# Performance work log

Measured on AMD Instinct MI355X. Metric: run time of the kernel, lower is better.

Reference implementation:

```python
import jax, jax.numpy as jnp
import numpy as np

N, E, IN_C, OUT_C, HEADS = 50000, 800000, 256, 256, 4
C = OUT_C // HEADS  # per-head channels = 64
BN_EPS = 1e-5


def setup_inputs() -> dict:
    key = jax.random.key(0)
    ks = jax.random.split(key, 16)
    inp = {
        'x': jax.random.normal(ks[0], (N, IN_C), dtype=jnp.float32),
        'edge_index': jax.random.randint(ks[1], (2, E), 0, N, dtype=jnp.int64),
        'edge_attr': jax.random.uniform(ks[2], (E, 1), dtype=jnp.float32),
        'spatial_coords': jax.random.normal(ks[3], (N, 2), dtype=jnp.float32),
        # GATConv params
        'W_gat': jax.random.normal(ks[4], (IN_C, HEADS * C), dtype=jnp.float32) * 0.05,
        'att_src': jax.random.normal(ks[5], (HEADS, C), dtype=jnp.float32) * 0.05,
        'att_dst': jax.random.normal(ks[6], (HEADS, C), dtype=jnp.float32) * 0.05,
        'bias_gat': jnp.zeros((HEADS * C,), dtype=jnp.float32),
        # spatial_attention MLP (computed but unused by the original forward)
        'w1': jax.random.normal(ks[7], (1, 64), dtype=jnp.float32) * 0.05,
        'b1': jnp.zeros((64,), dtype=jnp.float32),
        'w2': jax.random.normal(ks[8], (64, HEADS), dtype=jnp.float32) * 0.05,
        'b2': jnp.zeros((HEADS,), dtype=jnp.float32),
        # feature_transform: Linear + BatchNorm1d (eval stats) + ReLU (+Dropout=identity)
        'w_ft': jax.random.normal(ks[9], (IN_C, OUT_C), dtype=jnp.float32) * 0.05,
        'b_ft': jnp.zeros((OUT_C,), dtype=jnp.float32),
        'bn_gamma': jnp.ones((OUT_C,), dtype=jnp.float32),
        'bn_beta': jnp.zeros((OUT_C,), dtype=jnp.float32),
        'bn_mean': jax.random.normal(ks[10], (OUT_C,), dtype=jnp.float32) * 0.01,
        'bn_var': jax.random.uniform(ks[11], (OUT_C,), dtype=jnp.float32, minval=0.5, maxval=1.5),
    }
    return inp


def _forward(x, edge_index, edge_attr, W_gat, att_src, att_dst, bias_gat,
             w1, b1, w2, b2, w_ft, b_ft, bn_gamma, bn_beta, bn_mean, bn_var):
    n = x.shape[0]
    # add self-loops (PyG GATConv default)
    loop = jnp.arange(n, dtype=edge_index.dtype)
    src = jnp.concatenate([edge_index[0], loop])
    dst = jnp.concatenate([edge_index[1], loop])

    # linear transform: [N, heads, C]
    h = (x @ W_gat).reshape(n, HEADS, C)
    a_src = jnp.einsum('nhc,hc->nh', h, att_src)  # [N, H]
    a_dst = jnp.einsum('nhc,hc->nh', h, att_dst)  # [N, H]

    # per-edge attention logits, LeakyReLU(0.2)
    alpha = jax.nn.leaky_relu(a_src[src] + a_dst[dst], negative_slope=0.2)  # [Etot, H]
    # segment softmax over incoming edges of each destination node
    amax = jax.ops.segment_max(alpha, dst, num_segments=n)
    alpha = jnp.exp(alpha - amax[dst])
    denom = jax.ops.segment_sum(alpha, dst, num_segments=n)
    alpha = alpha / (denom[dst] + 1e-16)

    # weighted message aggregation
    msg = h[src] * alpha[:, :, None]                        # [Etot, H, C]
    agg = jax.ops.segment_sum(msg, dst, num_segments=n)     # [N, H, C]
    gat_out = agg.reshape(n, HEADS * C) + bias_gat

    # spatial attention weights (computed but UNUSED, matching original)
    spatial_weights = jax.nn.sigmoid(jax.nn.relu(edge_attr @ w1 + b1) @ w2 + b2)
    del spatial_weights

    # feature_transform (BatchNorm in eval mode, Dropout identity)
    y = x @ w_ft + b_ft
    y = (y - bn_mean) * jax.lax.rsqrt(bn_var + BN_EPS) * bn_gamma + bn_beta
    transformed = jax.nn.relu(y)

    return gat_out + transformed


def reference(x, edge_index, edge_attr, spatial_coords, W_gat, att_src, att_dst,
              bias_gat, w1, b1, w2, b2, w_ft, b_ft, bn_gamma, bn_beta, bn_mean, bn_var):
    # spatial_coords is accepted but unused by the original module's forward
    return _forward(x, edge_index, edge_attr, W_gat, att_src, att_dst, bias_gat,
                    w1, b1, w2, b2, w_ft, b_ft, bn_gamma, bn_beta, bn_mean, bn_var)
```

## Files before the change

kernel.cpp:

```cpp
#include <hip/hip_runtime.h>
#include <math.h>

typedef __attribute__((ext_vector_type(4))) float  f32x4;
typedef __attribute__((ext_vector_type(8))) short  short8;
typedef __attribute__((ext_vector_type(4))) unsigned short usx4;
typedef __attribute__((ext_vector_type(8))) unsigned short usx8;

__device__ __forceinline__ float bf2f(unsigned short u) {
    union { unsigned int i; float f; } c; c.i = ((unsigned int)u) << 16; return c.f;
}
__device__ __forceinline__ unsigned short f2bf(float f) {
    union { float f; unsigned int i; } c; c.f = f;
    unsigned int x = c.i;
    unsigned int r = (x + 0x7FFFu + ((x >> 16) & 1u)) >> 16;
    return (unsigned short)r;
}

__global__ __launch_bounds__(256) void k_convert_x(const float* __restrict__ x,
                                                   unsigned short* __restrict__ xb,
                                                   long total8) {
    long i = (long)blockIdx.x * blockDim.x + threadIdx.x;
    if (i >= total8) return;
    const f32x4* p = (const f32x4*)x;
    f32x4 v0 = p[2 * i], v1 = p[2 * i + 1];
    usx8 o;
    o[0] = f2bf(v0[0]); o[1] = f2bf(v0[1]); o[2] = f2bf(v0[2]); o[3] = f2bf(v0[3]);
    o[4] = f2bf(v1[0]); o[5] = f2bf(v1[1]); o[6] = f2bf(v1[2]); o[7] = f2bf(v1[3]);
    ((usx8*)xb)[i] = o;
}

__global__ __launch_bounds__(256) void k_convert_w(const float* __restrict__ Wg,
                                                   const float* __restrict__ Wf,
                                                   unsigned short* __restrict__ wbt) {
    int idx = blockIdx.x * blockDim.x + threadIdx.x;
    if (idx >= 512 * 256) return;
    int c = idx >> 8;
    int k = idx & 255;
    float v = (c < 256) ? Wg[k * 256 + c] : Wf[k * 256 + (c - 256)];
    wbt[idx] = f2bf(v);
}

#define BM 128
#define BN 128
#define BK 32
__global__ __launch_bounds__(256) void k_gemm(
    const float* __restrict__ x,
    const unsigned short* __restrict__ xb,
    const unsigned short* __restrict__ wbt,
    unsigned short* __restrict__ hb,
    unsigned short* __restrict__ tb,
    float* __restrict__ out,
    const float* __restrict__ b_ft, const float* __restrict__ bn_g,
    const float* __restrict__ bn_b, const float* __restrict__ bn_m,
    const float* __restrict__ bn_v, int M) {
    __shared__ unsigned short As[BM][BK + 8];
    __shared__ unsigned short Bs[BN][BK + 8];
    const int t = threadIdx.x;
    const int w = t >> 6, lane = t & 63;
    const int wr = w >> 1, wc = w & 1;
    const int bm0 = blockIdx.x * BM;
    const int bn0 = blockIdx.y * BN;
    const int kg = lane >> 4;
    const int lm = lane & 15;

    f32x4 acc[4][4] = {};

    for (int k0 = 0; k0 < 256; k0 += BK) {
        if (xb) {
            usx8 avv[2], bvv[2];
#pragma unroll
            for (int s = 0; s < 2; s++) {
                int seg = t + s * 256;
                int row = seg >> 2;
                int off = (seg & 3) * 8;
                int grow = bm0 + row; if (grow >= M) grow = M - 1;
                avv[s] = *(const usx8*)(xb + (long)grow * 256 + k0 + off);
                bvv[s] = *(const usx8*)(wbt + (long)(bn0 + row) * 256 + k0 + off);
            }
            __syncthreads();
#pragma unroll
            for (int s = 0; s < 2; s++) {
                int seg = t + s * 256;
                int row = seg >> 2;
                int off = (seg & 3) * 8;
                *(usx8*)&As[row][off] = avv[s];
                *(usx8*)&Bs[row][off] = bvv[s];
            }
        } else {
            f32x4 a0[2], a1[2];
            usx8 bv[2];
#pragma unroll
            for (int s = 0; s < 2; s++) {
                int seg = t + s * 256;
                int row = seg >> 2;
                int off = (seg & 3) * 8;
                int grow = bm0 + row; if (grow >= M) grow = M - 1;
                const float* ap = x + (long)grow * 256 + k0 + off;
                a0[s] = *(const f32x4*)ap;
                a1[s] = *(const f32x4*)(ap + 4);
                bv[s] = *(const usx8*)(wbt + (long)(bn0 + row) * 256 + k0 + off);
            }
            __syncthreads();
#pragma unroll
            for (int s = 0; s < 2; s++) {
                int seg = t + s * 256;
                int row = seg >> 2;
                int off = (seg & 3) * 8;
                usx8 av;
                av[0] = f2bf(a0[s][0]); av[1] = f2bf(a0[s][1]);
                av[2] = f2bf(a0[s][2]); av[3] = f2bf(a0[s][3]);
                av[4] = f2bf(a1[s][0]); av[5] = f2bf(a1[s][1]);
                av[6] = f2bf(a1[s][2]); av[7] = f2bf(a1[s][3]);
                *(usx8*)&As[row][off] = av;
                *(usx8*)&Bs[row][off] = bv[s];
            }
        }
        __syncthreads();
        short8 afr[4], bfr[4];
#pragma unroll
        for (int mi = 0; mi < 4; mi++)
            afr[mi] = *(const short8*)&As[wr * 64 + mi * 16 + lm][kg * 8];
#pragma unroll
        for (int nj = 0; nj < 4; nj++)
            bfr[nj] = *(const short8*)&Bs[wc * 64 + nj * 16 + lm][kg * 8];
#pragma unroll
        for (int mi = 0; mi < 4; mi++)
#pragma unroll
            for (int nj = 0; nj < 4; nj++)
                acc[mi][nj] = __builtin_amdgcn_mfma_f32_16x16x32_bf16(
                    afr[mi], bfr[nj], acc[mi][nj], 0, 0, 0);
        __syncthreads();
    }

    const bool isH = (bn0 < 256);
#pragma unroll
    for (int mi = 0; mi < 4; mi++) {
#pragma unroll
        for (int nj = 0; nj < 4; nj++) {
            int col = bn0 + wc * 64 + nj * 16 + lm;
            f32x4 a = acc[mi][nj];
            int rowbase = bm0 + wr * 64 + mi * 16 + kg * 4;
            if (isH) {
#pragma unroll
                for (int r = 0; r < 4; r++) {
                    int row = rowbase + r;
                    if (row < M) hb[(long)row * 256 + col] = f2bf(a[r]);
                }
            } else {
                int c2 = col - 256;
                float bft = b_ft[c2], mu = bn_m[c2];
                float iv = rsqrtf(bn_v[c2] + 1e-5f);
                float g = bn_g[c2], bt = bn_b[c2];
#pragma unroll
                for (int r = 0; r < 4; r++) {
                    int row = rowbase + r;
                    if (row < M) {
                        float v = (a[r] + bft - mu) * iv * g + bt;
                        v = v > 0.f ? v : 0.f;
                        if (tb) tb[(long)row * 256 + c2] = f2bf(v);
                        else    out[(long)row * 256 + c2] = v;
                    }
                }
            }
        }
    }
}

__global__ __launch_bounds__(256) void k_attn(const unsigned short* __restrict__ hb,
                                              const float* __restrict__ att_s,
                                              const float* __restrict__ att_d,
                                              float* __restrict__ a_src,
                                              float* __restrict__ a_dst, int N) {
    int gid = blockIdx.x * 256 + threadIdx.x;
    int node = gid >> 6;
    int lane = threadIdx.x & 63;
    if (node >= N) return;
    usx4 hv = ((const usx4*)(hb + (long)node * 256))[lane];
    int head = lane >> 4;
    int cb = (lane & 15) * 4;
    float s1 = 0.f, s2 = 0.f;
#pragma unroll
    for (int j = 0; j < 4; j++) {
        float h = bf2f(hv[j]);
        s1 += h * att_s[head * 64 + cb + j];
        s2 += h * att_d[head * 64 + cb + j];
    }
#pragma unroll
    for (int o = 1; o < 16; o <<= 1) {
        s1 += __shfl_xor(s1, o);
        s2 += __shfl_xor(s2, o);
    }
    if ((lane & 15) == 0) {
        a_src[node * 4 + head] = s1;
        a_dst[node * 4 + head] = s2;
    }
}

__global__ void k_count(const int* __restrict__ ei, int* __restrict__ deg,
                        int E, int N) {
    int i = blockIdx.x * blockDim.x + threadIdx.x;
    if (i >= E + N) return;
    int d = (i < E) ? ei[E + i] : (i - E);
    atomicAdd(&deg[d], 1);
}
__global__ __launch_bounds__(256) void k_scan1(const int* __restrict__ deg,
                                               int* __restrict__ offs,
                                               int* __restrict__ bsum, int n) {
    __shared__ int tmp[256];
    int b = blockIdx.x, t = threadIdx.x;
    int base = b * 1024;
    int v[4];
#pragma unroll
    for (int j = 0; j < 4; j++) {
        int i = base + t * 4 + j;
        v[j] = (i < n) ? deg[i] : 0;
    }
    int local = v[0] + v[1] + v[2] + v[3];
    tmp[t] = local;
    __syncthreads();
    for (int off = 1; off < 256; off <<= 1) {
        int xv = (t >= off) ? tmp[t - off] : 0;
        __syncthreads();
        tmp[t] += xv;
        __syncthreads();
    }
    int run = tmp[t] - local;
    if (t == 255) bsum[b] = tmp[255];
#pragma unroll
    for (int j = 0; j < 4; j++) {
        int i = base + t * 4 + j;
        if (i < n) offs[i] = run;
        run += v[j];
    }
}
__global__ void k_scan2(int* bsum, int nb) {
    if (threadIdx.x == 0 && blockIdx.x == 0) {
        int acc = 0;
        for (int i = 0; i < nb; i++) { int x = bsum[i]; bsum[i] = acc; acc += x; }
    }
}
__global__ void k_scan3(int* offs, const int* bsum, int n) {
    int i = blockIdx.x * blockDim.x + threadIdx.x;
    if (i < n) offs[i] += bsum[i >> 10];
}
__global__ void k_scatter(const int* __restrict__ ei, const int* __restrict__ offs,
                          int* __restrict__ cursor, int* __restrict__ srcs, int E, int N) {
    int i = blockIdx.x * blockDim.x + threadIdx.x;
    if (i >= E + N) return;
    int d, s;
    if (i < E) { d = ei[E + i]; s = ei[i]; }
    else       { d = i - E;     s = i - E; }
    int pos = atomicAdd(&cursor[d], 1);
    srcs[offs[d] + pos] = s;
}

__global__ __launch_bounds__(256) void k_agg(
    const int* __restrict__ offs, const int* __restrict__ srcs,
    const unsigned short* __restrict__ hb,
    const float* __restrict__ a_src, const float* __restrict__ a_dst,
    const float* __restrict__ bias_gat, const unsigned short* __restrict__ tb,
    float* __restrict__ out, int N, int E) {
    const int n = (blockIdx.x * 256 + threadIdx.x) >> 6;
    const int l = threadIdx.x & 63;
    if (n >= N) return;
    const int head = l >> 4;
    const int sub = l & 15;
    const int beg = offs[n];
    const int end = (n + 1 < N) ? offs[n + 1] : (E + N);

    const float ad = a_dst[(long)n * 4 + head];
    f32x4 acc = {};
    float den = 0.f;

    for (int base = beg; base < end; base += 16) {
        const int len = min(16, end - base);
        int sv = 0;
        float wsel = 0.f;
        if (base + sub < end) {
            sv = srcs[base + sub];
            float lv = a_src[(long)sv * 4 + head] + ad;
            lv = fmaxf(lv, 0.2f * lv);
            wsel = __expf(lv);
        }

#define AGG_EDGE(i)                                                        \
        {                                                                  \
            int src = __shfl(sv, (i));                                     \
            float wgt = __shfl(wsel, (l & 48) + (i));                      \
            uint2 hv = ((const uint2*)(hb + ((long)src << 8)))[l];         \
            den += wgt;                                                    \
            acc[0] = fmaf(wgt, __uint_as_float(hv.x << 16), acc[0]);       \
            acc[1] = fmaf(wgt, __uint_as_float(hv.x & 0xFFFF0000u), acc[1]);\
            acc[2] = fmaf(wgt, __uint_as_float(hv.y << 16), acc[2]);       \
            acc[3] = fmaf(wgt, __uint_as_float(hv.y & 0xFFFF0000u), acc[3]);\
        }

        if (len == 16) {
#pragma unroll
            for (int i = 0; i < 16; ++i) AGG_EDGE(i)
        } else {
            for (int i = 0; i < len; ++i) AGG_EDGE(i)
        }
#undef AGG_EDGE
    }

    const float inv = 1.f / (den + 1e-16f);
    const float4 bv = ((const float4*)bias_gat)[l];
    float4 trf;
    const long rowoff = ((long)n << 8) + l * 4;
    if (tb) {
        uint2 tv = ((const uint2*)(tb + ((long)n << 8)))[l];
        trf.x = __uint_as_float(tv.x << 16);
        trf.y = __uint_as_float(tv.x & 0xFFFF0000u);
        trf.z = __uint_as_float(tv.y << 16);
        trf.w = __uint_as_float(tv.y & 0xFFFF0000u);
    } else {
        trf = *(const float4*)(out + rowoff);
    }
    float4 r;
    r.x = acc[0] * inv + bv.x + trf.x;
    r.y = acc[1] * inv + bv.y + trf.y;
    r.z = acc[2] * inv + bv.z + trf.z;
    r.w = acc[3] * inv + bv.w + trf.w;
    *(float4*)(out + rowoff) = r;
}

extern "C" void kernel_launch(void* const* d_in, const int* in_sizes, int n_in,
                              void* d_out, int out_size, void* d_ws, size_t ws_size,
                              hipStream_t stream) {
    const float* x        = (const float*)d_in[0];
    const int*   ei       = (const int*)d_in[1];
    const float* W_gat    = (const float*)d_in[4];
    const float* att_src  = (const float*)d_in[5];
    const float* att_dst  = (const float*)d_in[6];
    const float* bias_gat = (const float*)d_in[7];
    const float* w_ft     = (const float*)d_in[12];
    const float* b_ft     = (const float*)d_in[13];
    const float* bn_g     = (const float*)d_in[14];
    const float* bn_b     = (const float*)d_in[15];
    const float* bn_m     = (const float*)d_in[16];
    const float* bn_v     = (const float*)d_in[17];
    float* out = (float*)d_out;

    const int N = in_sizes[0] / 256;
    const int E = in_sizes[1] / 2;
    const int ETOT = E + N;

    char* p = (char*)d_ws;
    char* pend = p + ws_size;
    auto alloc = [&](size_t bytes) {
        void* r = (void*)p;
        p += (bytes + 255) & ~(size_t)255;
        return r;
    };
    unsigned short* wbt  = (unsigned short*)alloc((size_t)512 * 256 * 2);
    unsigned short* hb   = (unsigned short*)alloc((size_t)N * 256 * 2);
    float* a_src = (float*)alloc((size_t)N * 4 * 4);
    float* a_dst = (float*)alloc((size_t)N * 4 * 4);
    int* deg    = (int*)alloc((size_t)N * 4);
    int* cursor = (int*)alloc((size_t)N * 4);
    int* offs   = (int*)alloc((size_t)(N + 1) * 4);
    int* bsum   = (int*)alloc((size_t)256 * 4);
    int* srcs   = (int*)alloc((size_t)ETOT * 4);
    unsigned short* xb = (unsigned short*)alloc((size_t)N * 256 * 2);
    if (p > pend) xb = nullptr;
    unsigned short* tb = (unsigned short*)alloc((size_t)N * 256 * 2);
    if (p > pend) tb = nullptr;

    k_convert_w<<<(512 * 256 + 255) / 256, 256, 0, stream>>>(W_gat, w_ft, wbt);
    if (xb) {
        long total8 = (long)N * 256 / 8;
        k_convert_x<<<(int)((total8 + 255) / 256), 256, 0, stream>>>(x, xb, total8);
    }

    dim3 gg((N + BM - 1) / BM, 4);
    k_gemm<<<gg, 256, 0, stream>>>(x, xb, wbt, hb, tb, out, b_ft, bn_g, bn_b, bn_m, bn_v, N);

    k_attn<<<(N + 3) / 4, 256, 0, stream>>>(hb, att_src, att_dst, a_src, a_dst, N);

    hipMemsetAsync(deg, 0, (((size_t)N * 4 + 255) & ~(size_t)255) + (size_t)N * 4, stream);
    k_count<<<(ETOT + 255) / 256, 256, 0, stream>>>(ei, deg, E, N);
    int nb = (N + 1023) / 1024;
    k_scan1<<<nb, 256, 0, stream>>>(deg, offs, bsum, N);
    k_scan2<<<1, 64, 0, stream>>>(bsum, nb);
    k_scan3<<<(N + 255) / 256, 256, 0, stream>>>(offs, bsum, N);
    k_scatter<<<(ETOT + 255) / 256, 256, 0, stream>>>(ei, offs, cursor, srcs, E, N);

    k_agg<<<(N * 64 + 255) / 256, 256, 0, stream>>>(offs, srcs, hb, a_src, a_dst,
                                                    bias_gat, tb, out, N, E);
}
```

Before: 251.6 us.

## Sort nodes by degree for aggregation, fuse x conversion into GEMM, swap grid axes

Builds a degree histogram, scans it in descending order and produces a node permutation, so the aggregation kernel processes high-degree nodes first and wavefronts in a block have similar degrees. This targets load imbalance and tail effects in the per-node gather loop. It also drops the separate fp32-to-bf16 conversion pass over x and converts inside the GEMM tile loads, and swaps the grid so the four N-tiles for one row block run next to each other and can share x in cache. It adds three small kernels and an indirection through perm, and output writes become scattered in node order.

```diff
diff --git a/kernel.cpp b/kernel.cpp
--- a/kernel.cpp
+++ b/kernel.cpp
@@ -14,19 +14,6 @@
     unsigned int x = c.i;
     unsigned int r = (x + 0x7FFFu + ((x >> 16) & 1u)) >> 16;
     return (unsigned short)r;
-}
-
-__global__ __launch_bounds__(256) void k_convert_x(const float* __restrict__ x,
-                                                   unsigned short* __restrict__ xb,
-                                                   long total8) {
-    long i = (long)blockIdx.x * blockDim.x + threadIdx.x;
-    if (i >= total8) return;
-    const f32x4* p = (const f32x4*)x;
-    f32x4 v0 = p[2 * i], v1 = p[2 * i + 1];
-    usx8 o;
-    o[0] = f2bf(v0[0]); o[1] = f2bf(v0[1]); o[2] = f2bf(v0[2]); o[3] = f2bf(v0[3]);
-    o[4] = f2bf(v1[0]); o[5] = f2bf(v1[1]); o[6] = f2bf(v1[2]); o[7] = f2bf(v1[3]);
-    ((usx8*)xb)[i] = o;
 }
 
 __global__ __launch_bounds__(256) void k_convert_w(const float* __restrict__ Wg,
@@ -45,7 +32,6 @@
 #define BK 32
 __global__ __launch_bounds__(256) void k_gemm(
     const float* __restrict__ x,
-    const unsigned short* __restrict__ xb,
     const unsigned short* __restrict__ wbt,
     unsigned short* __restrict__ hb,
     unsigned short* __restrict__ tb,
@@ -58,62 +44,40 @@
     const int t = threadIdx.x;
     const int w = t >> 6, lane = t & 63;
     const int wr = w >> 1, wc = w & 1;
-    const int bm0 = blockIdx.x * BM;
-    const int bn0 = blockIdx.y * BN;
+    const int bm0 = blockIdx.y * BM;
+    const int bn0 = blockIdx.x * BN;
     const int kg = lane >> 4;
     const int lm = lane & 15;
 
     f32x4 acc[4][4] = {};
 
     for (int k0 = 0; k0 < 256; k0 += BK) {
-        if (xb) {
-            usx8 avv[2], bvv[2];
-#pragma unroll
-            for (int s = 0; s < 2; s++) {
-                int seg = t + s * 256;
-                int row = seg >> 2;
-                int off = (seg & 3) * 8;
-                int grow = bm0 + row; if (grow >= M) grow = M - 1;
-                avv[s] = *(const usx8*)(xb + (long)grow * 256 + k0 + off);
-                bvv[s] = *(const usx8*)(wbt + (long)(bn0 + row) * 256 + k0 + off);
-            }
-            __syncthreads();
-#pragma unroll
-            for (int s = 0; s < 2; s++) {
-                int seg = t + s * 256;
-                int row = seg >> 2;
-                int off = (seg & 3) * 8;
-                *(usx8*)&As[row][off] = avv[s];
-                *(usx8*)&Bs[row][off] = bvv[s];
-            }
-        } else {
-            f32x4 a0[2], a1[2];
-            usx8 bv[2];
-#pragma unroll
-            for (int s = 0; s < 2; s++) {
-                int seg = t + s * 256;
-                int row = seg >> 2;
-                int off = (seg & 3) * 8;
-                int grow = bm0 + row; if (grow >= M) grow = M - 1;
-                const float* ap = x + (long)grow * 256 + k0 + off;
-                a0[s] = *(const f32x4*)ap;
-                a1[s] = *(const f32x4*)(ap + 4);
-                bv[s] = *(const usx8*)(wbt + (long)(bn0 + row) * 256 + k0 + off);
-            }
-            __syncthreads();
-#pragma unroll
-            for (int s = 0; s < 2; s++) {
-                int seg = t + s * 256;
-                int row = seg >> 2;
-                int off = (seg & 3) * 8;
-                usx8 av;
-                av[0] = f2bf(a0[s][0]); av[1] = f2bf(a0[s][1]);
-                av[2] = f2bf(a0[s][2]); av[3] = f2bf(a0[s][3]);
-                av[4] = f2bf(a1[s][0]); av[5] = f2bf(a1[s][1]);
-                av[6] = f2bf(a1[s][2]); av[7] = f2bf(a1[s][3]);
-                *(usx8*)&As[row][off] = av;
-                *(usx8*)&Bs[row][off] = bv[s];
-            }
+        f32x4 a0[2], a1[2];
+        usx8 bv[2];
+#pragma unroll
+        for (int s = 0; s < 2; s++) {
+            int seg = t + s * 256;
+            int row = seg >> 2;
+            int off = (seg & 3) * 8;
+            int grow = bm0 + row; if (grow >= M) grow = M - 1;
+            const float* ap = x + (long)grow * 256 + k0 + off;
+            a0[s] = *(const f32x4*)ap;
+            a1[s] = *(const f32x4*)(ap + 4);
+            bv[s] = *(const usx8*)(wbt + (long)(bn0 + row) * 256 + k0 + off);
+        }
+        __syncthreads();
+#pragma unroll
+        for (int s = 0; s < 2; s++) {
+            int seg = t + s * 256;
+            int row = seg >> 2;
+            int off = (seg & 3) * 8;
+            usx8 av;
+            av[0] = f2bf(a0[s][0]); av[1] = f2bf(a0[s][1]);
+            av[2] = f2bf(a0[s][2]); av[3] = f2bf(a0[s][3]);
+            av[4] = f2bf(a1[s][0]); av[5] = f2bf(a1[s][1]);
+            av[6] = f2bf(a1[s][2]); av[7] = f2bf(a1[s][3]);
+            *(usx8*)&As[row][off] = av;
+            *(usx8*)&Bs[row][off] = bv[s];
         }
         __syncthreads();
         short8 afr[4], bfr[4];
@@ -254,15 +218,44 @@
     srcs[offs[d] + pos] = s;
 }
 
+__global__ void k_hist(const int* __restrict__ deg, int* __restrict__ bins, int N) {
+    int i = blockIdx.x * blockDim.x + threadIdx.x;
+    if (i < N) atomicAdd(&bins[min(deg[i], 255)], 1);
+}
+__global__ __launch_bounds__(256) void k_binscan(int* __restrict__ bins) {
+    __shared__ int tmp[256];
+    int t = threadIdx.x;
+    int v = bins[t];
+    tmp[t] = v;
+    __syncthreads();
+    for (int off = 1; off < 256; off <<= 1) {
+        int xv = (t + off < 256) ? tmp[t + off] : 0;
+        __syncthreads();
+        tmp[t] += xv;
+        __syncthreads();
+    }
+    bins[t] = tmp[t] - v;
+}
+__global__ void k_perm(const int* __restrict__ deg, const int* __restrict__ bins,
+                       int* __restrict__ cur2, int* __restrict__ perm, int N) {
+    int i = blockIdx.x * blockDim.x + threadIdx.x;
+    if (i >= N) return;
+    int b = min(deg[i], 255);
+    int pos = atomicAdd(&cur2[b], 1);
+    perm[bins[b] + pos] = i;
+}
+
 __global__ __launch_bounds__(256) void k_agg(
+    const int* __restrict__ perm,
     const int* __restrict__ offs, const int* __restrict__ srcs,
     const unsigned short* __restrict__ hb,
     const float* __restrict__ a_src, const float* __restrict__ a_dst,
     const float* __restrict__ bias_gat, const unsigned short* __restrict__ tb,
     float* __restrict__ out, int N, int E) {
-    const int n = (blockIdx.x * 256 + threadIdx.x) >> 6;
+    const int gw = (blockIdx.x * 256 + threadIdx.x) >> 6;
     const int l = threadIdx.x & 63;
-    if (n >= N) return;
+    if (gw >= N) return;
+    const int n = perm[gw];
     const int head = l >> 4;
     const int sub = l & 15;
     const int beg = offs[n];
@@ -357,28 +350,27 @@
     unsigned short* hb   = (unsigned short*)alloc((size_t)N * 256 * 2);
     float* a_src = (float*)alloc((size_t)N * 4 * 4);
     float* a_dst = (float*)alloc((size_t)N * 4 * 4);
+    char* z0 = p;
     int* deg    = (int*)alloc((size_t)N * 4);
     int* cursor = (int*)alloc((size_t)N * 4);
+    int* bins   = (int*)alloc((size_t)256 * 4);
+    int* cur2   = (int*)alloc((size_t)256 * 4);
+    char* z1 = p;
     int* offs   = (int*)alloc((size_t)(N + 1) * 4);
     int* bsum   = (int*)alloc((size_t)256 * 4);
     int* srcs   = (int*)alloc((size_t)ETOT * 4);
-    unsigned short* xb = (unsigned short*)alloc((size_t)N * 256 * 2);
-    if (p > pend) xb = nullptr;
+    int* perm   = (int*)alloc((size_t)N * 4);
     unsigned short* tb = (unsigned short*)alloc((size_t)N * 256 * 2);
     if (p > pend) tb = nullptr;
 
     k_convert_w<<<(512 * 256 + 255) / 256, 256, 0, stream>>>(W_gat, w_ft, wbt);
-    if (xb) {
-        long total8 = (long)N * 256 / 8;
-        k_convert_x<<<(int)((total8 + 255) / 256), 256, 0, stream>>>(x, xb, total8);
-    }
-
-    dim3 gg((N + BM - 1) / BM, 4);
-    k_gemm<<<gg, 256, 0, stream>>>(x, xb, wbt, hb, tb, out, b_ft, bn_g, bn_b, bn_m, bn_v, N);
+
+    dim3 gg(4, (N + BM - 1) / BM);
+    k_gemm<<<gg, 256, 0, stream>>>(x, wbt, hb, tb, out, b_ft, bn_g, bn_b, bn_m, bn_v, N);
 
     k_attn<<<(N + 3) / 4, 256, 0, stream>>>(hb, att_src, att_dst, a_src, a_dst, N);
 
-    hipMemsetAsync(deg, 0, (((size_t)N * 4 + 255) & ~(size_t)255) + (size_t)N * 4, stream);
+    hipMemsetAsync(z0, 0, (size_t)(z1 - z0), stream);
     k_count<<<(ETOT + 255) / 256, 256, 0, stream>>>(ei, deg, E, N);
     int nb = (N + 1023) / 1024;
     k_scan1<<<nb, 256, 0, stream>>>(deg, offs, bsum, N);
@@ -386,6 +378,10 @@
     k_scan3<<<(N + 255) / 256, 256, 0, stream>>>(offs, bsum, N);
     k_scatter<<<(ETOT + 255) / 256, 256, 0, stream>>>(ei, offs, cursor, srcs, E, N);
 
-    k_agg<<<(N * 64 + 255) / 256, 256, 0, stream>>>(offs, srcs, hb, a_src, a_dst,
+    k_hist<<<(N + 255) / 256, 256, 0, stream>>>(deg, bins, N);
+    k_binscan<<<1, 256, 0, stream>>>(bins);
+    k_perm<<<(N + 255) / 256, 256, 0, stream>>>(deg, bins, cur2, perm, N);
+
+    k_agg<<<(N * 64 + 255) / 256, 256, 0, stream>>>(perm, offs, srcs, hb, a_src, a_dst,
                                                     bias_gat, tb, out, N, E);
 }
```

Result: slower. 557.5 us (+121.6%).
